# Kernel tuning notes

Measured on AMD Instinct MI355X. Metric: run time of the kernel, lower is better.

The kernel has to match this reference:

```python
import jax, jax.numpy as jnp
import numpy as np

V, C, L, H, N = 32000, 1024, 2, 16, 64
B, T, FF = 2, 1024, 4096
DW, DA, DV, DG = 64, 64, 32, 128


def setup_inputs() -> dict:
    ks = iter(jax.random.split(jax.random.key(0), 64))
    def nrm(shape, s=0.02):
        return jax.random.normal(next(ks), shape, jnp.float32) * s
    def uni(shape):
        return jax.random.uniform(next(ks), shape, jnp.float32)
    return dict(
        idx=jax.random.randint(next(ks), (B, T), 0, V, dtype=jnp.int32),
        emb_w=nrm((V, C)),
        ln0_g=jnp.ones((C,), jnp.float32), ln0_b=jnp.zeros((C,), jnp.float32),
        ln1_g=jnp.ones((L, C), jnp.float32), ln1_b=jnp.zeros((L, C), jnp.float32),
        ln2_g=jnp.ones((L, C), jnp.float32), ln2_b=jnp.zeros((L, C), jnp.float32),
        lnx_g=jnp.ones((L, C), jnp.float32), lnx_b=jnp.zeros((L, C), jnp.float32),
        lnout_g=jnp.ones((C,), jnp.float32), lnout_b=jnp.zeros((C,), jnp.float32),
        x_mix=uni((L, 6, C)),
        w0=nrm((L, C), 0.3) - 0.5,
        w1=nrm((L, C, DW)), w2=nrm((L, DW, C), 0.1),
        a0=jnp.zeros((L, C), jnp.float32), a1=nrm((L, C, DA)), a2=nrm((L, DA, C), 0.1),
        v0=jnp.ones((L, C), jnp.float32), v1=nrm((L, C, DV)), v2=nrm((L, DV, C), 0.1),
        g1=nrm((L, C, DG)), g2=nrm((L, DG, C), 0.1),
        k_k=jnp.full((L, C), 0.85, jnp.float32),
        k_a=jnp.ones((L, C), jnp.float32),
        r_k=nrm((L, H, N), 0.1),
        Wr=nrm((L, C, C)), Wk=nrm((L, C, C)), Wv=nrm((L, C, C)), Wo=nrm((L, C, C)),
        ffn_xk=uni((L, C)),
        ffn_k=nrm((L, C, FF)), ffn_v=nrm((L, FF, C)),
        time_state=nrm((L, H, N, N), 0.1),
        head_w=nrm((C, V)),
    )


def _ln(x, g, b, eps=1e-5):
    m = jnp.mean(x, -1, keepdims=True)
    v = jnp.mean(jnp.square(x - m), -1, keepdims=True)
    return (x - m) * jax.lax.rsqrt(v + eps) * g + b


def _shift(x):  # time_shift: prepend zero token, drop last
    return jnp.pad(x, ((0, 0), (1, 0), (0, 0)))[:, :-1]


def _rwkv7_scan(r, k, v, w, a, b, S0):
    # r,k,v,w,a,b: (B,T,H,N); S0: (B,H,N,N) laid out [value_dim, key_dim]
    # S_t = S_{t-1} * diag(exp(w_t)) + S_{t-1} a_t b_t^T + v_t k_t^T ; y_t = S_t r_t
    def step(S, inp):
        r_, k_, v_, w_, a_, b_ = inp
        sa = jnp.einsum('bhij,bhj->bhi', S, a_)
        S = (S * jnp.exp(w_)[:, :, None, :]
             + sa[..., None] * b_[:, :, None, :]
             + v_[..., None] * k_[:, :, None, :])
        y = jnp.einsum('bhij,bhj->bhi', S, r_)
        return S, y
    xs = tuple(jnp.moveaxis(t, 1, 0) for t in (r, k, v, w, a, b))
    S, ys = jax.lax.scan(step, S0, xs)
    return jnp.moveaxis(ys, 0, 1), S  # (B,T,H,N), (B,H,N,N)


def _forward(idx, emb_w, ln0_g, ln0_b, ln1_g, ln1_b, ln2_g, ln2_b, lnx_g, lnx_b,
             lnout_g, lnout_b, x_mix, w0, w1, w2, a0, a1, a2, v0, v1, v2,
             g1, g2, k_k, k_a, r_k, Wr, Wk, Wv, Wo, ffn_xk, ffn_k, ffn_v,
             time_state, head_w):
    Bv, Tv = idx.shape
    Lh, Hh, Nh = r_k.shape
    x = emb_w[idx]                      # (B,T,C)
    v_first = jnp.zeros_like(x)
    for i in range(Lh):
        if i == 0:
            x = _ln(x, ln0_g, ln0_b)
        xin = _ln(x, ln1_g[i], ln1_b[i])
        xx = _shift(xin) - xin
        xr, xw, xk, xv, xa_, xg = (xin + xx * x_mix[i, j] for j in range(6))
        r = xr @ Wr[i]
        w = -jax.nn.softplus(-(w0[i] + jnp.tanh(xw @ w1[i]) @ w2[i])) - 0.5
        k = xk @ Wk[i]
        v = xv @ Wv[i]
        if i == 0:
            v_first = v
        else:
            v = v + (v_first - v) * jax.nn.sigmoid(v0[i] + (xv @ v1[i]) @ v2[i])
        a = jax.nn.sigmoid(a0[i] + (xa_ @ a1[i]) @ a2[i])
        g = jax.nn.sigmoid(xg @ g1[i]) @ g2[i]
        kk = (k * k_k[i]).reshape(Bv, Tv, Hh, Nh)
        kk = kk / jnp.maximum(jnp.linalg.norm(kk, axis=-1, keepdims=True), 1e-12)
        kk = kk.reshape(Bv, Tv, -1)
        k2 = k * (1.0 + (a - 1.0) * k_a[i])
        rs = lambda t: t.reshape(Bv, Tv, Hh, Nh)
        S0 = jnp.broadcast_to(time_state[i], (Bv, Hh, Nh, Nh))
        y, _S = _rwkv7_scan(rs(r), rs(k2), rs(v), rs(w), rs(-kk), rs(kk * a), S0)
        # ln_x = GroupNorm(H, C, eps=64e-5): per-head normalization
        m = y.mean(-1, keepdims=True)
        var = jnp.square(y - m).mean(-1, keepdims=True)
        y = (y - m) * jax.lax.rsqrt(var + 64e-5)
        y = y * lnx_g[i].reshape(Hh, Nh) + lnx_b[i].reshape(Hh, Nh)
        bonus = (rs(r) * rs(k2) * r_k[i]).sum(-1, keepdims=True) * rs(v)
        y = (y + bonus).reshape(Bv, Tv, -1)
        x = x + (y * g) @ Wo[i]
        # channel mix (x070 FFN)
        xc = _ln(x, ln2_g[i], ln2_b[i])
        kx = xc + (_shift(xc) - xc) * ffn_xk[i]
        x = x + jnp.square(jax.nn.relu(kx @ ffn_k[i])) @ ffn_v[i]
    return _ln(x, lnout_g, lnout_b) @ head_w


def reference(idx, emb_w, ln0_g, ln0_b, ln1_g, ln1_b, ln2_g, ln2_b, lnx_g, lnx_b,
              lnout_g, lnout_b, x_mix, w0, w1, w2, a0, a1, a2, v0, v1, v2,
              g1, g2, k_k, k_a, r_k, Wr, Wk, Wv, Wo, ffn_xk, ffn_k, ffn_v,
              time_state, head_w):
    return _forward(idx, emb_w, ln0_g, ln0_b, ln1_g, ln1_b, ln2_g, ln2_b,
                    lnx_g, lnx_b, lnout_g, lnout_b, x_mix, w0, w1, w2,
                    a0, a1, a2, v0, v1, v2, g1, g2, k_k, k_a, r_k,
                    Wr, Wk, Wv, Wo, ffn_xk, ffn_k, ffn_v, time_state, head_w)
```

## Files before the change

kernel.cpp:

```cpp
#include <hip/hip_runtime.h>
#include <hip/hip_bf16.h>
#include <math.h>

#define V_  32000
#define C_  1024
#define L_  2
#define H_  16
#define N_  64
#define B_  2
#define T_  1024
#define FF_ 4096
#define DW_ 64
#define DA_ 64
#define DV_ 32
#define DG_ 128
#define BT_  (B_*T_)
#define BTC_ (BT_*C_)

typedef float floatx4 __attribute__((ext_vector_type(4)));
typedef short shortx8 __attribute__((ext_vector_type(8)));
typedef __attribute__((address_space(1))) unsigned int gu32;
typedef __attribute__((address_space(3))) unsigned int su32;

__device__ __forceinline__ float sigf(float x){ return 1.0f/(1.0f+expf(-x)); }
__device__ __forceinline__ unsigned short f2bf(float x){
  __hip_bfloat16 h = __float2bfloat16(x);
  return *(unsigned short*)&h;
}
__device__ __forceinline__ void gload16(const void* g, void* l){
  __builtin_amdgcn_global_load_lds((const gu32*)g, (su32*)l, 16, 0, 0);
}

__device__ __forceinline__ float dpp_red16(float s){
  s += __int_as_float(__builtin_amdgcn_update_dpp(0, __float_as_int(s), 0xB1, 0xf, 0xf, true));
  s += __int_as_float(__builtin_amdgcn_update_dpp(0, __float_as_int(s), 0x4E, 0xf, 0xf, true));
  s += __int_as_float(__builtin_amdgcn_update_dpp(0, __float_as_int(s), 0x141, 0xf, 0xf, true));
  s += __int_as_float(__builtin_amdgcn_update_dpp(0, __float_as_int(s), 0x140, 0xf, 0xf, true));
  return s;
}

__global__ void k_embed(const int* __restrict__ idx, const float* __restrict__ emb,
                        float* __restrict__ x){
  int i = blockIdx.x*256 + threadIdx.x;
  if (i >= BTC_) return;
  int row = i / C_, c = i - row*C_;
  x[i] = emb[(size_t)idx[row]*C_ + c];
}

__global__ void k_ln(const float* __restrict__ x, const float* __restrict__ g,
                     const float* __restrict__ b, float* __restrict__ out,
                     unsigned short* __restrict__ out16){
  int row = blockIdx.x;
  const float* xr = x + (size_t)row*C_;
  float s = 0.f, s2 = 0.f;
  for (int c = threadIdx.x; c < C_; c += 256){ float v = xr[c]; s += v; s2 += v*v; }
  for (int o = 32; o > 0; o >>= 1){ s += __shfl_xor(s,o); s2 += __shfl_xor(s2,o); }
  __shared__ float w1s[4], w2s[4];
  int wid = threadIdx.x >> 6, lane = threadIdx.x & 63;
  if (lane == 0){ w1s[wid] = s; w2s[wid] = s2; }
  __syncthreads();
  if (threadIdx.x == 0){
    float a = 0.f, bb = 0.f;
    for (int i = 0; i < 4; i++){ a += w1s[i]; bb += w2s[i]; }
    w1s[0] = a; w2s[0] = bb;
  }
  __syncthreads();
  float mean = w1s[0] * (1.0f/C_);
  float var  = w2s[0] * (1.0f/C_) - mean*mean;
  float r = rsqrtf(var + 1e-5f);
  if (out16){
    unsigned short* orow = out16 + (size_t)row*C_;
    for (int c = threadIdx.x; c < C_; c += 256)
      orow[c] = f2bf((xr[c]-mean)*r*g[c] + b[c]);
  } else {
    float* orow = out + (size_t)row*C_;
    for (int c = threadIdx.x; c < C_; c += 256)
      orow[c] = (xr[c]-mean)*r*g[c] + b[c];
  }
}

__global__ void k_lnmix(const float* __restrict__ x, const float* __restrict__ g,
                        const float* __restrict__ b, const float* __restrict__ mixl,
                        unsigned short* __restrict__ m6){
  int row = blockIdx.x;
  int t = row & (T_-1);
  const float* xr = x + (size_t)row*C_;
  const float* xp = xr - C_;
  float s0=0.f,q0=0.f,s1=0.f,q1=0.f;
  for (int c = threadIdx.x; c < C_; c += 256){
    float v = xr[c]; s0 += v; q0 += v*v;
    if (t > 0){ float u = xp[c]; s1 += u; q1 += u*u; }
  }
  for (int o=32;o>0;o>>=1){
    s0+=__shfl_xor(s0,o); q0+=__shfl_xor(q0,o);
    s1+=__shfl_xor(s1,o); q1+=__shfl_xor(q1,o);
  }
  __shared__ float rA[4], rB[4], rC[4], rD[4];
  int wid = threadIdx.x>>6, lane = threadIdx.x&63;
  if (lane==0){ rA[wid]=s0; rB[wid]=q0; rC[wid]=s1; rD[wid]=q1; }
  __syncthreads();
  if (threadIdx.x==0){
    float a=0,bb=0,cc=0,dd=0;
    for(int i=0;i<4;i++){a+=rA[i];bb+=rB[i];cc+=rC[i];dd+=rD[i];}
    rA[0]=a;rB[0]=bb;rC[0]=cc;rD[0]=dd;
  }
  __syncthreads();
  float m0 = rA[0]*(1.f/C_);
  float r0 = rsqrtf(rB[0]*(1.f/C_)-m0*m0 + 1e-5f);
  float m1=0.f, r1=0.f;
  if (t>0){ m1 = rC[0]*(1.f/C_); r1 = rsqrtf(rD[0]*(1.f/C_)-m1*m1 + 1e-5f); }
  size_t base = (size_t)row*C_;
  for (int c = threadIdx.x; c < C_; c += 256){
    float cur = (xr[c]-m0)*r0*g[c]+b[c];
    float pv  = (t>0) ? (xp[c]-m1)*r1*g[c]+b[c] : 0.f;
    float d = pv - cur;
#pragma unroll
    for (int j=0;j<6;j++)
      m6[(size_t)j*BTC_ + base + c] = f2bf(cur + d*mixl[j*C_+c]);
  }
}

__global__ void k_lnffn(const float* __restrict__ x, const float* __restrict__ g,
                        const float* __restrict__ b, const float* __restrict__ fxk,
                        unsigned short* __restrict__ kx){
  int row = blockIdx.x;
  int t = row & (T_-1);
  const float* xr = x + (size_t)row*C_;
  const float* xp = xr - C_;
  float s0=0.f,q0=0.f,s1=0.f,q1=0.f;
  for (int c = threadIdx.x; c < C_; c += 256){
    float v = xr[c]; s0 += v; q0 += v*v;
    if (t > 0){ float u = xp[c]; s1 += u; q1 += u*u; }
  }
  for (int o=32;o>0;o>>=1){
    s0+=__shfl_xor(s0,o); q0+=__shfl_xor(q0,o);
    s1+=__shfl_xor(s1,o); q1+=__shfl_xor(q1,o);
  }
  __shared__ float rA[4], rB[4], rC[4], rD[4];
  int wid = threadIdx.x>>6, lane = threadIdx.x&63;
  if (lane==0){ rA[wid]=s0; rB[wid]=q0; rC[wid]=s1; rD[wid]=q1; }
  __syncthreads();
  if (threadIdx.x==0){
    float a=0,bb=0,cc=0,dd=0;
    for(int i=0;i<4;i++){a+=rA[i];bb+=rB[i];cc+=rC[i];dd+=rD[i];}
    rA[0]=a;rB[0]=bb;rC[0]=cc;rD[0]=dd;
  }
  __syncthreads();
  float m0 = rA[0]*(1.f/C_);
  float r0 = rsqrtf(rB[0]*(1.f/C_)-m0*m0 + 1e-5f);
  float m1=0.f, r1=0.f;
  if (t>0){ m1 = rC[0]*(1.f/C_); r1 = rsqrtf(rD[0]*(1.f/C_)-m1*m1 + 1e-5f); }
  size_t base = (size_t)row*C_;
  for (int c = threadIdx.x; c < C_; c += 256){
    float cur = (xr[c]-m0)*r0*g[c]+b[c];
    float pv  = (t>0) ? (xp[c]-m1)*r1*g[c]+b[c] : 0.f;
    kx[base + c] = f2bf(cur + (pv - cur)*fxk[c]);
  }
}

__global__ void k_kk(const float* __restrict__ kkw, const float* __restrict__ kaw,
                     const float* __restrict__ a, float* __restrict__ k,
                     float* __restrict__ kk, float* __restrict__ bba){
  int bth = blockIdx.x;
  int lane = threadIdx.x;
  int bt = bth / H_, h = bth - bt*H_;
  int cix = h*N_ + lane;
  size_t gi = (size_t)bt*C_ + cix;
  float kv = k[gi];
  float kkv = kv * kkw[cix];
  float ss = kkv*kkv;
  for (int o = 32; o > 0; o >>= 1) ss += __shfl_xor(ss,o);
  float nrm = fmaxf(sqrtf(ss), 1e-12f);
  float kkn = kkv / nrm;
  kk[gi] = kkn;
  float av = a[gi];
  bba[gi] = -kkn*av;
  k[gi] = kv * (1.f + (av - 1.f)*kaw[cix]);
}

#define SCHUNK 16
#define SROWS  8
__global__ __launch_bounds__(128) void k_scan(
    const float* __restrict__ r, const float* __restrict__ k2,
    const float* __restrict__ v, const float* __restrict__ wd,
    const float* __restrict__ kk, const float* __restrict__ bba,
    const float* __restrict__ S0, float* __restrict__ y){
  int bh = blockIdx.x & 31;
  int rblk = blockIdx.x >> 5;
  int b = bh / H_, h = bh - b*H_;
  int tid = threadIdx.x;
  int wave = tid >> 6, lane = tid & 63;
  int rg = tid >> 4;
  int row = rblk*SROWS + rg;
  int cg = tid & 15;
  int c0 = cg*4;

  __shared__ __attribute__((aligned(16))) float buf[2][6][SCHUNK][64];

  float S[4];
  {
    const floatx4 s0 = *(const floatx4*)&S0[((size_t)h*N_ + row)*N_ + c0];
#pragma unroll
    for (int ci = 0; ci < 4; ci++) S[ci] = s0[ci];
  }

  size_t hoff = ((size_t)b*T_)*C_ + (size_t)h*N_;

  auto do_stage = [&](int t0, int bi){
#pragma unroll
    for (int q = 0; q < 12; q++){
      int u = wave*12 + q;
      int vec = u >> 2, tt4 = (u & 3)*4;
      int tt = tt4 + (lane >> 4);
      const float* src;
      switch (vec){
        case 0: src = r;   break;
        case 1: src = k2;  break;
        case 2: src = v;   break;
        case 3: src = wd;  break;
        case 4: src = kk;  break;
        default: src = bba; break;
      }
      src += hoff + (size_t)(t0 + tt)*C_ + (size_t)((lane & 15)*4);
      gload16(src, &buf[bi][vec][tt4][0]);
    }
  };

  do_stage(0, 0);
  asm volatile("s_waitcnt vmcnt(0)" ::: "memory");
  __builtin_amdgcn_s_barrier();

  const int NC = T_/SCHUNK;
  size_t off = hoff;
  for (int c = 0; c < NC; c++){
    int bi = c & 1;
    bool more = (c + 1 < NC);
    if (more) do_stage((c+1)*SCHUNK, bi ^ 1);
    asm volatile("" ::: "memory");

    floatx4 rv  = *(const floatx4*)&buf[bi][0][0][c0];
    floatx4 kv  = *(const floatx4*)&buf[bi][1][0][c0];
    float   vi  = buf[bi][2][0][row];
    floatx4 dd  = *(const floatx4*)&buf[bi][3][0][c0];
    floatx4 kkv = *(const floatx4*)&buf[bi][4][0][c0];
    floatx4 bav = *(const floatx4*)&buf[bi][5][0][c0];
#pragma unroll
    for (int tt = 0; tt < SCHUNK; tt++, off += C_){
      floatx4 rv2, kv2, dd2, kkv2, bav2; float vi2;
      if (tt + 1 < SCHUNK){
        rv2  = *(const floatx4*)&buf[bi][0][tt+1][c0];
        kv2  = *(const floatx4*)&buf[bi][1][tt+1][c0];
        vi2  = buf[bi][2][tt+1][row];
        dd2  = *(const floatx4*)&buf[bi][3][tt+1][c0];
        kkv2 = *(const floatx4*)&buf[bi][4][tt+1][c0];
        bav2 = *(const floatx4*)&buf[bi][5][tt+1][c0];
      }
      float s = S[0]*kkv[0];
      s = fmaf(S[1], kkv[1], s);
      s = fmaf(S[2], kkv[2], s);
      s = fmaf(S[3], kkv[3], s);
      float sa = dpp_red16(s);
      float yy = 0.f;
#pragma unroll
      for (int ci = 0; ci < 4; ci++){
        float t0v = fmaf(vi, kv[ci], sa*bav[ci]);
        float sn = fmaf(S[ci], dd[ci], t0v);
        S[ci] = sn;
        yy = fmaf(sn, rv[ci], yy);
      }
      float yv = dpp_red16(yy);
      if (cg == 0) y[off + row] = yv;
      if (tt + 1 < SCHUNK){
        rv = rv2; kv = kv2; vi = vi2; dd = dd2; kkv = kkv2; bav = bav2;
      }
    }
    if (more){
      asm volatile("s_waitcnt vmcnt(16)" ::: "memory");
      __builtin_amdgcn_sched_barrier(0);
      __builtin_amdgcn_s_barrier();
    }
  }
}

__global__ void k_gnb(const float* __restrict__ lxg, const float* __restrict__ lxb,
                      const float* __restrict__ rk, const float* __restrict__ r,
                      const float* __restrict__ k2, const float* __restrict__ v,
                      const float* __restrict__ g, const float* __restrict__ y,
                      unsigned short* __restrict__ yg){
  int bth = blockIdx.x;
  int lane = threadIdx.x;
  int bt = bth / H_, h = bth - bt*H_;
  int cix = h*N_ + lane;
  size_t gi = (size_t)bt*C_ + cix;
  float yv = y[gi];
  float s = yv;
  for (int o = 32; o > 0; o >>= 1) s += __shfl_xor(s,o);
  float mean = s * (1.0f/N_);
  float d = yv - mean;
  float s2 = d*d;
  for (int o = 32; o > 0; o >>= 1) s2 += __shfl_xor(s2,o);
  float var = s2 * (1.0f/N_);
  float yn = d * rsqrtf(var + 64e-5f) * lxg[cix] + lxb[cix];
  float dv = r[gi]*k2[gi]*rk[h*N_ + lane];
  for (int o = 32; o > 0; o >>= 1) dv += __shfl_xor(dv,o);
  yg[gi] = f2bf((yn + dv*v[gi]) * g[gi]);
}

__global__ void k_tc(const float* __restrict__ in, unsigned short* __restrict__ out,
                     int R, int Cc, int Cpad){
  __shared__ float t[32][33];
  int c0 = blockIdx.x*32, r0 = blockIdx.y*32;
  int tx = threadIdx.x, ty = threadIdx.y;
  for (int i = ty; i < 32; i += 8){
    int r = r0+i, c = c0+tx;
    t[i][tx] = (r < R && c < Cc) ? in[(size_t)r*Cc + c] : 0.f;
  }
  __syncthreads();
  for (int i = ty; i < 32; i += 8){
    int oc = c0+i, orr = r0+tx;
    if (oc < Cpad && orr < R) out[(size_t)oc*R + orr] = f2bf(t[tx][i]);
  }
}

__global__ __launch_bounds__(256) void k_mgemm(
    const short* __restrict__ A, int lda, const short* __restrict__ Bt,
    float* __restrict__ Cf, unsigned short* __restrict__ Cb, int ldc,
    int K, int ep, const float* __restrict__ ec, const float* __restrict__ e1){
  __shared__ __attribute__((aligned(16))) short As[128*32];
  __shared__ __attribute__((aligned(16))) short Bs[128*32];
  int m0 = blockIdx.y*128, n0 = blockIdx.x*128;
  int tid = threadIdx.x, wave = tid >> 6, lane = tid & 63;
  int lhi = lane >> 4, llo = lane & 15;
  int wm = wave & 1, wn = wave >> 1;
  int arow = lane >> 2, acol = (lane & 3)*8;
  floatx4 acc[4][4];
#pragma unroll
  for (int i = 0; i < 4; i++)
#pragma unroll
    for (int j = 0; j < 4; j++) acc[i][j] = (floatx4){0.f,0.f,0.f,0.f};

  for (int k0 = 0; k0 < K; k0 += 32){
#pragma unroll
    for (int q = 0; q < 2; q++){
      int r0 = wave*32 + q*16;
      gload16(A  + (size_t)(m0 + r0 + arow)*lda + k0 + acol, As + r0*32);
      gload16(Bt + (size_t)(n0 + r0 + arow)*K   + k0 + acol, Bs + r0*32);
    }
    __syncthreads();
    shortx8 af[4], bfv[4];
#pragma unroll
    for (int mi = 0; mi < 4; mi++)
      af[mi] = *(const shortx8*)(As + ((wm*64 + mi*16 + llo)*32 + lhi*8));
#pragma unroll
    for (int nj = 0; nj < 4; nj++)
      bfv[nj] = *(const shortx8*)(Bs + ((wn*64 + nj*16 + llo)*32 + lhi*8));
#pragma unroll
    for (int mi = 0; mi < 4; mi++)
#pragma unroll
      for (int nj = 0; nj < 4; nj++)
        acc[mi][nj] = __builtin_amdgcn_mfma_f32_16x16x32_bf16(af[mi], bfv[nj], acc[mi][nj], 0, 0, 0);
    __syncthreads();
  }
#pragma unroll
  for (int mi = 0; mi < 4; mi++){
#pragma unroll
    for (int nj = 0; nj < 4; nj++){
      int gr0 = m0 + wm*64 + mi*16 + lhi*4;
      int gc  = n0 + wn*64 + nj*16 + llo;
#pragma unroll
      for (int rg = 0; rg < 4; rg++){
        size_t ci = (size_t)(gr0 + rg)*ldc + gc;
        float v = acc[mi][nj][rg];
        switch (ep){
          case 0: Cf[ci] = v; break;
          case 1: Cf[ci] += v; break;
          case 2: Cb[ci] = f2bf(v); break;
          case 3: Cb[ci] = f2bf(tanhf(v)); break;
          case 4: Cb[ci] = f2bf(sigf(v)); break;
          case 5: { float rr = fmaxf(v, 0.f); Cb[ci] = f2bf(rr*rr); } break;
          case 6: Cf[ci] = sigf(ec[gc] + v) * 0.60653065971263342f; break;
          case 7: Cf[ci] = sigf(ec[gc] + v); break;
          case 8: { float sg = sigf(ec[gc] + v); float cv = Cf[ci];
                    Cf[ci] = cv + (e1[ci] - cv)*sg; } break;
        }
      }
    }
  }
}

extern "C" void kernel_launch(void* const* d_in, const int* in_sizes, int n_in,
                              void* d_out, int out_size, void* d_ws, size_t ws_size,
                              hipStream_t stream){
  const int*   idx     = (const int*)  d_in[0];
  const float* emb_w   = (const float*)d_in[1];
  const float* ln0_g   = (const float*)d_in[2];
  const float* ln0_b   = (const float*)d_in[3];
  const float* ln1_g   = (const float*)d_in[4];
  const float* ln1_b   = (const float*)d_in[5];
  const float* ln2_g   = (const float*)d_in[6];
  const float* ln2_b   = (const float*)d_in[7];
  const float* lnx_g   = (const float*)d_in[8];
  const float* lnx_b   = (const float*)d_in[9];
  const float* lnout_g = (const float*)d_in[10];
  const float* lnout_b = (const float*)d_in[11];
  const float* x_mix   = (const float*)d_in[12];
  const float* w0      = (const float*)d_in[13];
  const float* w1      = (const float*)d_in[14];
  const float* w2      = (const float*)d_in[15];
  const float* a0      = (const float*)d_in[16];
  const float* a1      = (const float*)d_in[17];
  const float* a2      = (const float*)d_in[18];
  const float* v0      = (const float*)d_in[19];
  const float* v1      = (const float*)d_in[20];
  const float* v2      = (const float*)d_in[21];
  const float* g1      = (const float*)d_in[22];
  const float* g2      = (const float*)d_in[23];
  const float* k_k     = (const float*)d_in[24];
  const float* k_a     = (const float*)d_in[25];
  const float* r_k     = (const float*)d_in[26];
  const float* Wr      = (const float*)d_in[27];
  const float* Wk      = (const float*)d_in[28];
  const float* Wv      = (const float*)d_in[29];
  const float* Wo      = (const float*)d_in[30];
  const float* ffn_xk  = (const float*)d_in[31];
  const float* ffn_k   = (const float*)d_in[32];
  const float* ffn_v   = (const float*)d_in[33];
  const float* tstate  = (const float*)d_in[34];
  const float* head_w  = (const float*)d_in[35];
  float* out = (float*)d_out;

  char* p = (char*)d_ws;
  auto alloc = [&](size_t bytes)->void*{ void* r = (void*)p; p += (bytes + 255) & ~(size_t)255; return r; };
  float* x      = (float*)alloc((size_t)BTC_*4);
  float* vfirst = (float*)alloc((size_t)BTC_*4);
  float* xin    = (float*)alloc((size_t)BTC_*4);
  float* rb     = (float*)alloc((size_t)BTC_*4);
  float* wdec   = (float*)alloc((size_t)BTC_*4);
  float* kb     = (float*)alloc((size_t)BTC_*4);
  float* vb     = (float*)alloc((size_t)BTC_*4);
  float* ab     = (float*)alloc((size_t)BTC_*4);
  float* kkb    = (float*)alloc((size_t)BTC_*4);
  float* yb     = (float*)alloc((size_t)BTC_*4);
  float* gb     = (float*)alloc((size_t)BTC_*4);
  unsigned short* act16 = (unsigned short*)alloc((size_t)6*BTC_*2);
  unsigned short* m_r = act16;
  unsigned short* m_w = act16 + 1*(size_t)BTC_;
  unsigned short* m_k = act16 + 2*(size_t)BTC_;
  unsigned short* m_v = act16 + 3*(size_t)BTC_;
  unsigned short* m_a = act16 + 4*(size_t)BTC_;
  unsigned short* m_g = act16 + 5*(size_t)BTC_;
  unsigned short* yg16  = m_r;
  unsigned short* kx16  = m_w;
  unsigned short* hid16 = m_k;
  unsigned short* xh16  = m_r;
  unsigned short* w16 = (unsigned short*)alloc((size_t)BT_*128*2);
  unsigned short* a16 = (unsigned short*)alloc((size_t)BT_*128*2);
  unsigned short* v16 = (unsigned short*)alloc((size_t)BT_*128*2);
  unsigned short* g16 = (unsigned short*)alloc((size_t)BT_*128*2);
  unsigned short *WrT[L_], *WkT[L_], *WvT[L_], *WoT[L_];
  unsigned short *w1T[L_], *a1T[L_], *v1T[L_], *g1T[L_];
  unsigned short *w2T[L_], *a2T[L_], *v2T[L_], *g2T[L_];
  unsigned short *fkT[L_], *fvT[L_];
  for (int l = 0; l < L_; l++){
    WrT[l] = (unsigned short*)alloc((size_t)C_*C_*2);
    WkT[l] = (unsigned short*)alloc((size_t)C_*C_*2);
    WvT[l] = (unsigned short*)alloc((size_t)C_*C_*2);
    WoT[l] = (unsigned short*)alloc((size_t)C_*C_*2);
    w1T[l] = (unsigned short*)alloc((size_t)128*C_*2);
    a1T[l] = (unsigned short*)alloc((size_t)128*C_*2);
    v1T[l] = (unsigned short*)alloc((size_t)128*C_*2);
    g1T[l] = (unsigned short*)alloc((size_t)128*C_*2);
    w2T[l] = (unsigned short*)alloc((size_t)C_*64*2);
    a2T[l] = (unsigned short*)alloc((size_t)C_*64*2);
    v2T[l] = (unsigned short*)alloc((size_t)C_*32*2);
    g2T[l] = (unsigned short*)alloc((size_t)C_*128*2);
    fkT[l] = (unsigned short*)alloc((size_t)FF_*C_*2);
    fvT[l] = (unsigned short*)alloc((size_t)C_*FF_*2);
  }
  unsigned short* hwT = (unsigned short*)alloc((size_t)V_*C_*2);

  dim3 blk(256);
  dim3 tcb(32, 8);

  auto MG = [&](const unsigned short* A, int lda, const unsigned short* Bt,
                float* Cf, unsigned short* Cb, int ldc, int M, int Nn, int K, int ep,
                const float* ec = 0, const float* e1 = 0){
    k_mgemm<<<dim3(Nn/128, M/128), 256, 0, stream>>>(
      (const short*)A, lda, (const short*)Bt, Cf, Cb, ldc, K, ep, ec, e1);
  };

  for (int l = 0; l < L_; l++){
    k_tc<<<dim3(32,32), tcb, 0, stream>>>(Wr + (size_t)l*C_*C_, WrT[l], C_, C_, C_);
    k_tc<<<dim3(32,32), tcb, 0, stream>>>(Wk + (size_t)l*C_*C_, WkT[l], C_, C_, C_);
    k_tc<<<dim3(32,32), tcb, 0, stream>>>(Wv + (size_t)l*C_*C_, WvT[l], C_, C_, C_);
    k_tc<<<dim3(32,32), tcb, 0, stream>>>(Wo + (size_t)l*C_*C_, WoT[l], C_, C_, C_);
    k_tc<<<dim3(4,32),  tcb, 0, stream>>>(w1 + (size_t)l*C_*DW_, w1T[l], C_, DW_, 128);
    k_tc<<<dim3(4,32),  tcb, 0, stream>>>(a1 + (size_t)l*C_*DA_, a1T[l], C_, DA_, 128);
    k_tc<<<dim3(4,32),  tcb, 0, stream>>>(v1 + (size_t)l*C_*DV_, v1T[l], C_, DV_, 128);
    k_tc<<<dim3(4,32),  tcb, 0, stream>>>(g1 + (size_t)l*C_*DG_, g1T[l], C_, DG_, 128);
    k_tc<<<dim3(32,2),  tcb, 0, stream>>>(w2 + (size_t)l*DW_*C_, w2T[l], DW_, C_, C_);
    k_tc<<<dim3(32,2),  tcb, 0, stream>>>(a2 + (size_t)l*DA_*C_, a2T[l], DA_, C_, C_);
    k_tc<<<dim3(32,1),  tcb, 0, stream>>>(v2 + (size_t)l*DV_*C_, v2T[l], DV_, C_, C_);
    k_tc<<<dim3(32,4),  tcb, 0, stream>>>(g2 + (size_t)l*DG_*C_, g2T[l], DG_, C_, C_);
    k_tc<<<dim3(128,32),tcb, 0, stream>>>(ffn_k + (size_t)l*C_*FF_, fkT[l], C_, FF_, FF_);
    k_tc<<<dim3(32,128),tcb, 0, stream>>>(ffn_v + (size_t)l*FF_*C_, fvT[l], FF_, C_, C_);
  }
  k_tc<<<dim3(1000,32), tcb, 0, stream>>>(head_w, hwT, C_, V_, V_);

  int ewg = (BTC_ + 255)/256;
  k_embed<<<ewg, blk, 0, stream>>>(idx, emb_w, x);

  for (int l = 0; l < L_; l++){
    const float* mixl = x_mix + ((size_t)l*6)*C_;
    if (l == 0)
      k_ln<<<BT_, blk, 0, stream>>>(x, ln0_g, ln0_b, x, (unsigned short*)0);
    k_lnmix<<<BT_, blk, 0, stream>>>(x, ln1_g + l*C_, ln1_b + l*C_, mixl, act16);

    MG(m_r, C_, WrT[l], rb, 0, C_, BT_, C_, C_, 0);
    MG(m_w, C_, w1T[l], 0, w16, 128, BT_, 128, C_, 3);
    MG(m_k, C_, WkT[l], kb, 0, C_, BT_, C_, C_, 0);
    MG(m_v, C_, WvT[l], vb, 0, C_, BT_, C_, C_, 0);
    if (l > 0)
      MG(m_v, C_, v1T[l], 0, v16, 128, BT_, 128, C_, 2);
    MG(m_a, C_, a1T[l], 0, a16, 128, BT_, 128, C_, 2);
    MG(m_g, C_, g1T[l], 0, g16, 128, BT_, 128, C_, 4);

    MG(w16, 128, w2T[l], wdec, 0, C_, BT_, C_, DW_, 6, w0 + l*C_);
    MG(a16, 128, a2T[l], ab,   0, C_, BT_, C_, DA_, 7, a0 + l*C_);
    if (l == 0){
      hipMemcpyAsync(vfirst, vb, (size_t)BTC_*4, hipMemcpyDeviceToDevice, stream);
    } else {
      MG(v16, 128, v2T[l], vb, 0, C_, BT_, C_, DV_, 8, v0 + l*C_, vfirst);
    }
    MG(g16, 128, g2T[l], gb, 0, C_, BT_, C_, DG_, 0);

    k_kk<<<BT_*H_, 64, 0, stream>>>(k_k + l*C_, k_a + l*C_, ab, kb, kkb, xin);

    k_scan<<<B_*H_*(N_/SROWS), 128, 0, stream>>>(rb, kb, vb, wdec, kkb, xin,
                                      tstate + (size_t)l*H_*N_*N_, yb);

    k_gnb<<<BT_*H_, 64, 0, stream>>>(lnx_g + l*C_, lnx_b + l*C_, r_k + (size_t)l*H_*N_,
                                     rb, kb, vb, gb, yb, yg16);

    MG(yg16, C_, WoT[l], x, 0, C_, BT_, C_, C_, 1);

    k_lnffn<<<BT_, blk, 0, stream>>>(x, ln2_g + l*C_, ln2_b + l*C_, ffn_xk + l*C_, kx16);
    MG(kx16, C_, fkT[l], 0, hid16, FF_, BT_, FF_, C_, 5);
    MG(hid16, FF_, fvT[l], x, 0, C_, BT_, C_, FF_, 1);
  }

  k_ln<<<BT_, blk, 0, stream>>>(x, lnout_g, lnout_b, (float*)0, xh16);
  MG(xh16, C_, hwT, out, 0, V_, BT_, V_, C_, 0);
}
```

Baseline: 2.640 ms.

## Swizzle GEMM LDS tiles, template epilogue, and swap grid order

XOR-swizzles the 16-byte column chunks of the A and B tiles in shared memory so that the fragment reads hit different LDS banks instead of conflicting ones. The epilogue selector becomes a template parameter, so each instantiation drops the runtime switch and the unused code paths. The grid axes are also swapped so that consecutive blocks walk along M, which changes how B tiles are reused in L2. It adds nine kernel instantiations, and the swizzle has to stay consistent between the global-to-LDS load and the fragment reads.

```diff
diff --git a/kernel.cpp b/kernel.cpp
--- a/kernel.cpp
+++ b/kernel.cpp
@@ -322,17 +322,20 @@
   }
 }
 
+template<int EP>
 __global__ __launch_bounds__(256) void k_mgemm(
     const short* __restrict__ A, int lda, const short* __restrict__ Bt,
     float* __restrict__ Cf, unsigned short* __restrict__ Cb, int ldc,
-    int K, int ep, const float* __restrict__ ec, const float* __restrict__ e1){
+    int K, const float* __restrict__ ec, const float* __restrict__ e1){
   __shared__ __attribute__((aligned(16))) short As[128*32];
   __shared__ __attribute__((aligned(16))) short Bs[128*32];
-  int m0 = blockIdx.y*128, n0 = blockIdx.x*128;
+  int m0 = blockIdx.x*128, n0 = blockIdx.y*128;
   int tid = threadIdx.x, wave = tid >> 6, lane = tid & 63;
   int lhi = lane >> 4, llo = lane & 15;
   int wm = wave & 1, wn = wave >> 1;
-  int arow = lane >> 2, acol = (lane & 3)*8;
+  int arow = lane >> 2;
+  int scol = ((lane & 3) ^ ((arow >> 1) & 3)) * 8;
+  int swz  = (llo >> 1) & 3;
   floatx4 acc[4][4];
 #pragma unroll
   for (int i = 0; i < 4; i++)
@@ -343,17 +346,17 @@
 #pragma unroll
     for (int q = 0; q < 2; q++){
       int r0 = wave*32 + q*16;
-      gload16(A  + (size_t)(m0 + r0 + arow)*lda + k0 + acol, As + r0*32);
-      gload16(Bt + (size_t)(n0 + r0 + arow)*K   + k0 + acol, Bs + r0*32);
+      gload16(A  + (size_t)(m0 + r0 + arow)*lda + k0 + scol, As + r0*32);
+      gload16(Bt + (size_t)(n0 + r0 + arow)*K   + k0 + scol, Bs + r0*32);
     }
     __syncthreads();
     shortx8 af[4], bfv[4];
 #pragma unroll
     for (int mi = 0; mi < 4; mi++)
-      af[mi] = *(const shortx8*)(As + ((wm*64 + mi*16 + llo)*32 + lhi*8));
+      af[mi] = *(const shortx8*)(As + ((wm*64 + mi*16 + llo)*32 + (lhi^swz)*8));
 #pragma unroll
     for (int nj = 0; nj < 4; nj++)
-      bfv[nj] = *(const shortx8*)(Bs + ((wn*64 + nj*16 + llo)*32 + lhi*8));
+      bfv[nj] = *(const shortx8*)(Bs + ((wn*64 + nj*16 + llo)*32 + (lhi^swz)*8));
 #pragma unroll
     for (int mi = 0; mi < 4; mi++)
 #pragma unroll
@@ -371,18 +374,16 @@
       for (int rg = 0; rg < 4; rg++){
         size_t ci = (size_t)(gr0 + rg)*ldc + gc;
         float v = acc[mi][nj][rg];
-        switch (ep){
-          case 0: Cf[ci] = v; break;
-          case 1: Cf[ci] += v; break;
-          case 2: Cb[ci] = f2bf(v); break;
-          case 3: Cb[ci] = f2bf(tanhf(v)); break;
-          case 4: Cb[ci] = f2bf(sigf(v)); break;
-          case 5: { float rr = fmaxf(v, 0.f); Cb[ci] = f2bf(rr*rr); } break;
-          case 6: Cf[ci] = sigf(ec[gc] + v) * 0.60653065971263342f; break;
-          case 7: Cf[ci] = sigf(ec[gc] + v); break;
-          case 8: { float sg = sigf(ec[gc] + v); float cv = Cf[ci];
-                    Cf[ci] = cv + (e1[ci] - cv)*sg; } break;
-        }
+        if constexpr (EP == 0) Cf[ci] = v;
+        else if constexpr (EP == 1) Cf[ci] += v;
+        else if constexpr (EP == 2) Cb[ci] = f2bf(v);
+        else if constexpr (EP == 3) Cb[ci] = f2bf(tanhf(v));
+        else if constexpr (EP == 4) Cb[ci] = f2bf(sigf(v));
+        else if constexpr (EP == 5) { float rr = fmaxf(v, 0.f); Cb[ci] = f2bf(rr*rr); }
+        else if constexpr (EP == 6) Cf[ci] = sigf(ec[gc] + v) * 0.60653065971263342f;
+        else if constexpr (EP == 7) Cf[ci] = sigf(ec[gc] + v);
+        else if constexpr (EP == 8) { float sg = sigf(ec[gc] + v); float cv = Cf[ci];
+                                      Cf[ci] = cv + (e1[ci] - cv)*sg; }
       }
     }
   }
@@ -485,8 +486,19 @@
   auto MG = [&](const unsigned short* A, int lda, const unsigned short* Bt,
                 float* Cf, unsigned short* Cb, int ldc, int M, int Nn, int K, int ep,
                 const float* ec = 0, const float* e1 = 0){
-    k_mgemm<<<dim3(Nn/128, M/128), 256, 0, stream>>>(
-      (const short*)A, lda, (const short*)Bt, Cf, Cb, ldc, K, ep, ec, e1);
+    dim3 g(M/128, Nn/128);
+    const short* As_ = (const short*)A; const short* Bs_ = (const short*)Bt;
+    switch (ep){
+      case 0: k_mgemm<0><<<g,256,0,stream>>>(As_,lda,Bs_,Cf,Cb,ldc,K,ec,e1); break;
+      case 1: k_mgemm<1><<<g,256,0,stream>>>(As_,lda,Bs_,Cf,Cb,ldc,K,ec,e1); break;
+      case 2: k_mgemm<2><<<g,256,0,stream>>>(As_,lda,Bs_,Cf,Cb,ldc,K,ec,e1); break;
+      case 3: k_mgemm<3><<<g,256,0,stream>>>(As_,lda,Bs_,Cf,Cb,ldc,K,ec,e1); break;
+      case 4: k_mgemm<4><<<g,256,0,stream>>>(As_,lda,Bs_,Cf,Cb,ldc,K,ec,e1); break;
+      case 5: k_mgemm<5><<<g,256,0,stream>>>(As_,lda,Bs_,Cf,Cb,ldc,K,ec,e1); break;
+      case 6: k_mgemm<6><<<g,256,0,stream>>>(As_,lda,Bs_,Cf,Cb,ldc,K,ec,e1); break;
+      case 7: k_mgemm<7><<<g,256,0,stream>>>(As_,lda,Bs_,Cf,Cb,ldc,K,ec,e1); break;
+      case 8: k_mgemm<8><<<g,256,0,stream>>>(As_,lda,Bs_,Cf,Cb,ldc,K,ec,e1); break;
+    }
   };
 
   for (int l = 0; l < L_; l++){
```

Result: faster. 2.138 ms (-19.0%).
